# Optimization experiments

Hardware: AMD Instinct MI355X
Metric: run time of the kernel (lower is better)

The kernel has to match this reference:

```python
import jax, jax.numpy as jnp
import numpy as np
import math

D_MODEL = 1024
N_HEAD = 16
D_HEAD = D_MODEL // N_HEAD
B, T = 4, 2048


def setup_inputs() -> dict:
    key = jax.random.key(0)
    ks = jax.random.split(key, 9)
    x = jax.random.normal(ks[0], (B, T, D_MODEL), dtype=jnp.float32)
    # causal mask, broadcastable to [B, H, T, T]; mask==0 -> -1e9
    mask = jnp.tril(jnp.ones((T, T), dtype=bool))[None, None, :, :]
    # Xavier-uniform linear weights (stored as [in, out] for x @ W), zero biases
    limit = math.sqrt(6.0 / (D_MODEL + D_MODEL))
    def w(k):
        return jax.random.uniform(k, (D_MODEL, D_MODEL), dtype=jnp.float32, minval=-limit, maxval=limit)
    return {
        "x": x,
        "mask": mask,
        "wq": w(ks[1]), "bq": jnp.zeros((D_MODEL,), jnp.float32),
        "wk": w(ks[2]), "bk": jnp.zeros((D_MODEL,), jnp.float32),
        "wv": w(ks[3]), "bv": jnp.zeros((D_MODEL,), jnp.float32),
        "wo": w(ks[4]), "bo": jnp.zeros((D_MODEL,), jnp.float32),
    }


def reference(x, mask, wq, bq, wk, bk, wv, bv, wo, bo):
    b, t, c = x.shape
    h, dh = N_HEAD, D_HEAD
    # [B,T,C] -> [B,H,T,dh]
    def heads(y):
        return y.reshape(b, t, h, dh).transpose(0, 2, 1, 3)
    q = heads(x @ wq + bq)
    k = heads(x @ wk + bk)
    v = heads(x @ wv + bv)
    att = jnp.einsum("bhqd,bhkd->bhqk", q, k) / math.sqrt(dh)
    att = jnp.where(mask, att, jnp.float32(-1e9))
    att = jax.nn.softmax(att, axis=-1)  # dropout is identity in eval mode
    out = jnp.einsum("bhqk,bhkd->bhqd", att, v)
    out = out.transpose(0, 2, 1, 3).reshape(b, t, c)
    return out @ wo + bo
```

## Files before the change

kernel.cpp:

```cpp
#include <hip/hip_runtime.h>

typedef __bf16 bf16_t;
typedef bf16_t bf16x8 __attribute__((ext_vector_type(8)));
typedef bf16_t bf16x4 __attribute__((ext_vector_type(4)));
typedef float  f32x4  __attribute__((ext_vector_type(4)));
typedef float  f32x16 __attribute__((ext_vector_type(16)));
typedef unsigned int u32;
typedef u32 u32x2 __attribute__((ext_vector_type(2)));
typedef u32 u32x4 __attribute__((ext_vector_type(4)));

#define T_SEQ 2048
#define C_DIM 1024
#define NH    16
#define DH    64
#define BATCH 4
#define M_TOK (BATCH * T_SEQ)

#define Q_SCALE 0.1803368801111137f
#define DEFER_THR 8.0f

#define AS1 __attribute__((address_space(1)))
#define AS3 __attribute__((address_space(3)))

__device__ __forceinline__ void gld_lds16(const bf16_t* g, bf16_t* l) {
  __builtin_amdgcn_global_load_lds(
      (const AS1 u32*)(uintptr_t)g,
      (AS3 u32*)(u32)(uintptr_t)l, 16, 0, 0);
}

__device__ __forceinline__ void plswap(u32& a, u32& b) {
  u32x2 r = __builtin_amdgcn_permlane32_swap(a, b, false, false);
  a = r[0]; b = r[1];
}
__device__ __forceinline__ float xmax32(float x) {
  u32 a = __builtin_bit_cast(u32, x), b = a;
  plswap(a, b);
  return fmaxf(__builtin_bit_cast(float, a), __builtin_bit_cast(float, b));
}
__device__ __forceinline__ float xsum32(float x) {
  u32 a = __builtin_bit_cast(u32, x), b = a;
  plswap(a, b);
  return __builtin_bit_cast(float, a) + __builtin_bit_cast(float, b);
}

__global__ __launch_bounds__(256) void msa_cvt_x(const float* __restrict__ x,
                                                 bf16_t* __restrict__ xb, int n4) {
  int i = blockIdx.x * 256 + threadIdx.x;
  if (i < n4) {
    const float4 v = ((const float4*)x)[i];
    bf16x4 o;
    o[0] = (bf16_t)v.x; o[1] = (bf16_t)v.y; o[2] = (bf16_t)v.z; o[3] = (bf16_t)v.w;
    ((bf16x4*)xb)[i] = o;
  }
}

__global__ __launch_bounds__(256) void msa_transpose_w(
    const float* __restrict__ wq, const float* __restrict__ wk,
    const float* __restrict__ wv, const float* __restrict__ wo,
    bf16_t* __restrict__ wt_qkv, bf16_t* __restrict__ wt_o) {
  __shared__ float tile[32][33];
  const int a = blockIdx.z;
  const float* src = (a == 0) ? wq : (a == 1) ? wk : (a == 2) ? wv : wo;
  bf16_t* dst = (a < 3) ? (wt_qkv + (size_t)a * C_DIM * C_DIM) : wt_o;
  const int tx = threadIdx.x & 31, ty = threadIdx.x >> 5;
  const int bi = blockIdx.y * 32, bj = blockIdx.x * 32;
#pragma unroll
  for (int p = 0; p < 4; p++) {
    int r = p * 8 + ty;
    tile[r][tx] = src[(size_t)(bi + r) * C_DIM + bj + tx];
  }
  __syncthreads();
#pragma unroll
  for (int p = 0; p < 4; p++) {
    int r = p * 8 + ty;
    dst[(size_t)(bj + r) * C_DIM + bi + tx] = (bf16_t)tile[tx][r];
  }
}

__global__ __launch_bounds__(256) void msa_gemm_qkv(
    const bf16_t* __restrict__ xb, const bf16_t* __restrict__ wt,
    const float* __restrict__ bq, const float* __restrict__ bk,
    const float* __restrict__ bv,
    bf16_t* __restrict__ qo, bf16_t* __restrict__ ko, bf16_t* __restrict__ vto) {
  __shared__ bf16_t lA[2 * 128 * 32];
  __shared__ bf16_t lB[2 * 128 * 32];
  const int tid = threadIdx.x;
  const int w = tid >> 6, lane = tid & 63;
  const int lr = lane & 15, lg = lane >> 4;
  const int m0 = blockIdx.y * 128;
  const int n0 = blockIdx.x * 128;
  const int wm = (w >> 1) * 64, wn = (w & 1) * 64;

  const int srow = tid >> 2, scol = (tid & 3) * 8;
  const bf16_t* ga = xb + (size_t)(m0 + srow) * C_DIM + scol;
  const bf16_t* gb = wt + (size_t)(n0 + srow) * C_DIM + scol;

  f32x4 acc[4][4];
#pragma unroll
  for (int i = 0; i < 4; i++)
#pragma unroll
    for (int j = 0; j < 4; j++) acc[i][j] = (f32x4){0.f, 0.f, 0.f, 0.f};

  for (int k0 = 0; k0 < C_DIM; k0 += 64) {
    gld_lds16(ga + k0, &lA[tid * 8]);
    gld_lds16(ga + (size_t)64 * C_DIM + k0, &lA[2048 + tid * 8]);
    gld_lds16(ga + k0 + 32, &lA[4096 + tid * 8]);
    gld_lds16(ga + (size_t)64 * C_DIM + k0 + 32, &lA[6144 + tid * 8]);
    gld_lds16(gb + k0, &lB[tid * 8]);
    gld_lds16(gb + (size_t)64 * C_DIM + k0, &lB[2048 + tid * 8]);
    gld_lds16(gb + k0 + 32, &lB[4096 + tid * 8]);
    gld_lds16(gb + (size_t)64 * C_DIM + k0 + 32, &lB[6144 + tid * 8]);
    __syncthreads();
#pragma unroll
    for (int h = 0; h < 2; h++) {
      bf16x8 a[4], b[4];
#pragma unroll
      for (int mb = 0; mb < 4; mb++)
        a[mb] = *(const bf16x8*)&lA[h * 4096 + (wm + mb * 16 + lr) * 32 + lg * 8];
#pragma unroll
      for (int nb = 0; nb < 4; nb++)
        b[nb] = *(const bf16x8*)&lB[h * 4096 + (wn + nb * 16 + lr) * 32 + lg * 8];
#pragma unroll
      for (int mb = 0; mb < 4; mb++)
#pragma unroll
        for (int nb = 0; nb < 4; nb++)
          acc[mb][nb] = __builtin_amdgcn_mfma_f32_16x16x32_bf16(a[mb], b[nb], acc[mb][nb], 0, 0, 0);
    }
    __syncthreads();
  }

#pragma unroll
  for (int nb = 0; nb < 4; nb++) {
    const int n = n0 + wn + nb * 16 + lr;
    const int g = n >> 10, c = n & 1023, h = c >> 6, d = c & 63;
    const float bias = (g == 0) ? bq[c] : (g == 1) ? bk[c] : bv[c];
#pragma unroll
    for (int mb = 0; mb < 4; mb++) {
#pragma unroll
      for (int r = 0; r < 4; r++) {
        const int m = m0 + wm + mb * 16 + lg * 4 + r;
        const int bi = m >> 11, t = m & (T_SEQ - 1);
        float v = acc[mb][nb][r] + bias;
        if (g == 0)
          qo[(((size_t)bi * NH + h) * T_SEQ + t) * DH + d] = (bf16_t)(v * Q_SCALE);
        else if (g == 1)
          ko[(((size_t)bi * NH + h) * T_SEQ + t) * DH + d] = (bf16_t)v;
        else
          vto[(((size_t)bi * NH + h) * DH + d) * T_SEQ + t] = (bf16_t)v;
      }
    }
  }
}

__device__ __forceinline__ void pack_frag(const f32x16& s, bf16x8& pa0, bf16x8& pa1) {
  u32 pk8[8];
#pragma unroll
  for (int i = 0; i < 8; i++) {
    const unsigned short lo = __builtin_bit_cast(unsigned short, (bf16_t)s[2 * i]);
    const unsigned short hh = __builtin_bit_cast(unsigned short, (bf16_t)s[2 * i + 1]);
    pk8[i] = ((u32)hh << 16) | (u32)lo;
  }
  u32 f0w0 = pk8[0], f0w2 = pk8[2];
  u32 f0w1 = pk8[1], f0w3 = pk8[3];
  u32 f1w0 = pk8[4], f1w2 = pk8[6];
  u32 f1w1 = pk8[5], f1w3 = pk8[7];
  plswap(f0w0, f0w2);
  plswap(f0w1, f0w3);
  plswap(f1w0, f1w2);
  plswap(f1w1, f1w3);
  const u32x4 q0v = {f0w0, f0w1, f0w2, f0w3};
  const u32x4 q1v = {f1w0, f1w1, f1w2, f1w3};
  pa0 = __builtin_bit_cast(bf16x8, q0v);
  pa1 = __builtin_bit_cast(bf16x8, q1v);
}

__device__ __forceinline__ void sm_pack(f32x16& s, float& m_run, float& l_run,
                                        f32x16& o0, f32x16& o1,
                                        bf16x8& pa0, bf16x8& pa1) {
  float t0 = fmaxf(fmaxf(s[0], s[1]), s[2]);
  float t1 = fmaxf(fmaxf(s[3], s[4]), s[5]);
  float t2 = fmaxf(fmaxf(s[6], s[7]), s[8]);
  float t3 = fmaxf(fmaxf(s[9], s[10]), s[11]);
  float t4 = fmaxf(fmaxf(s[12], s[13]), s[14]);
  float t5 = fmaxf(fmaxf(t0, t1), s[15]);
  float mt = fmaxf(fmaxf(fmaxf(t2, t3), t4), t5);
  mt = xmax32(mt);

  if (__any(mt > m_run + DEFER_THR)) {
    const float mnew = fmaxf(m_run, mt);
    const float al = __builtin_amdgcn_exp2f(m_run - mnew);
    m_run = mnew;
    l_run *= al;
#pragma unroll
    for (int r = 0; r < 16; r++) { o0[r] *= al; o1[r] *= al; }
  }

#pragma unroll
  for (int r = 0; r < 16; r++) s[r] = __builtin_amdgcn_exp2f(s[r] - m_run);
  {
    float a0 = (s[0] + s[1]) + (s[2] + s[3]);
    float a1 = (s[4] + s[5]) + (s[6] + s[7]);
    float a2 = (s[8] + s[9]) + (s[10] + s[11]);
    float a3 = (s[12] + s[13]) + (s[14] + s[15]);
    l_run += xsum32((a0 + a1) + (a2 + a3));
  }
  pack_frag(s, pa0, pa1);
}

__device__ __forceinline__ void store_o(f32x16& o0, f32x16& o1, float l_fin,
                                        bf16_t* __restrict__ orow, const int hi) {
  const float inv = 1.0f / l_fin;
#pragma unroll
  for (int db = 0; db < 2; db++) {
#pragma unroll
    for (int r = 0; r < 16; r += 2) {
      const int d = db * 32 + (r & 3) + 8 * (r >> 2) + 4 * hi;
      const float v0 = (db ? o1[r] : o0[r]) * inv;
      const float v1 = (db ? o1[r + 1] : o0[r + 1]) * inv;
      const unsigned short b0 = __builtin_bit_cast(unsigned short, (bf16_t)v0);
      const unsigned short b1 = __builtin_bit_cast(unsigned short, (bf16_t)v1);
      *reinterpret_cast<u32*>(orow + d) = ((u32)b1 << 16) | (u32)b0;
    }
  }
}

__global__ __launch_bounds__(256, 2) void msa_attn_lds(
    const bf16_t* __restrict__ Q, const bf16_t* __restrict__ K,
    const bf16_t* __restrict__ Vt, bf16_t* __restrict__ O) {
  __shared__ __align__(16) char lds[16384];
  const int tid = threadIdx.x;
  const int w = tid >> 6;
  const int lane = tid & 63;
  const int l31 = lane & 31;
  const int hi = lane >> 5;
  const int bh = blockIdx.x;
  const int pg = blockIdx.y;
  const int p = pg * 4 + w;
  const int tS = p, tL = 63 - p;
  const int q0S = tS * 32, q0L = tL * 32;
  const int KT_MAX = 63 - 4 * pg;

  const bf16_t* Qh = Q + (size_t)bh * T_SEQ * DH;
  const bf16_t* Kh = K + (size_t)bh * T_SEQ * DH;
  const bf16_t* Vh = Vt + (size_t)bh * DH * T_SEQ;

  bf16x8 qfL[4], qfS[4];
#pragma unroll
  for (int dc = 0; dc < 4; dc++) {
    qfL[dc] = *(const bf16x8*)(Qh + (size_t)(q0L + l31) * DH + dc * 16 + hi * 8);
    qfS[dc] = *(const bf16x8*)(Qh + (size_t)(q0S + l31) * DH + dc * 16 + hi * 8);
  }

  f32x16 oL0, oL1, oS0, oS1;
#pragma unroll
  for (int r = 0; r < 16; r++) { oL0[r] = 0.f; oL1[r] = 0.f; oS0[r] = 0.f; oS1[r] = 0.f; }
  float mL = -1e30f, lL = 0.f, mS = -1e30f, lS = 0.f;
  const f32x16 z16 = {};

  const int ksw = (l31 & 7) << 4;
  const int vsw = (l31 & 3) << 4;
  const int krow = tid >> 3;
  const int kce = ((16 * (tid & 7)) ^ ((krow & 7) << 4)) >> 1;
  const int vrow = tid >> 2;
  const int vce = ((16 * (tid & 3)) ^ ((vrow & 3) << 4)) >> 1;

#define STAGE(KT, BUF)                                                         \
  {                                                                            \
    const int jj = (KT) * 32;                                                  \
    bf16_t* base_ = (bf16_t*)(lds + (BUF) * 8192);                             \
    gld_lds16(Kh + (size_t)(jj + krow) * DH + kce, base_ + tid * 8);           \
    gld_lds16(Vh + (size_t)vrow * T_SEQ + jj + vce, base_ + 2048 + tid * 8);   \
  }

  STAGE(0, 0);
  __syncthreads();

  for (int kt = 0; kt <= KT_MAX; ++kt) {
    const int buf = kt & 1;
    if (kt < KT_MAX) STAGE(kt + 1, buf ^ 1);

    const bool doL = (kt <= tL);
    if (doL) {
      const char* kb = lds + buf * 8192;
      const char* vb = kb + 4096;
      bf16x8 kf[4];
#pragma unroll
      for (int dc = 0; dc < 4; dc++)
        kf[dc] = *(const bf16x8*)(kb + l31 * 128 + ((dc * 32 + hi * 16) ^ ksw));
      const bf16x8 vf00 = *(const bf16x8*)(vb + l31 * 64 + ((hi * 16) ^ vsw));
      const bf16x8 vf01 = *(const bf16x8*)(vb + l31 * 64 + ((32 + hi * 16) ^ vsw));
      const bf16x8 vf10 = *(const bf16x8*)(vb + (32 + l31) * 64 + ((hi * 16) ^ vsw));
      const bf16x8 vf11 = *(const bf16x8*)(vb + (32 + l31) * 64 + ((32 + hi * 16) ^ vsw));

      const bool doS = (kt <= tS);
      f32x16 sL = __builtin_amdgcn_mfma_f32_32x32x16_bf16(kf[0], qfL[0], z16, 0, 0, 0);
#pragma unroll
      for (int dc = 1; dc < 4; dc++)
        sL = __builtin_amdgcn_mfma_f32_32x32x16_bf16(kf[dc], qfL[dc], sL, 0, 0, 0);
      f32x16 sS;
      if (doS) {
        sS = __builtin_amdgcn_mfma_f32_32x32x16_bf16(kf[0], qfS[0], z16, 0, 0, 0);
#pragma unroll
        for (int dc = 1; dc < 4; dc++)
          sS = __builtin_amdgcn_mfma_f32_32x32x16_bf16(kf[dc], qfS[dc], sS, 0, 0, 0);
      }
      if (kt == tL) {
#pragma unroll
        for (int r = 0; r < 16; r++) {
          const int jrow = (r & 3) + 8 * (r >> 2) + 4 * hi;
          if (jrow > l31) sL[r] = -1e30f;
        }
      }
      if (kt == tS) {
#pragma unroll
        for (int r = 0; r < 16; r++) {
          const int jrow = (r & 3) + 8 * (r >> 2) + 4 * hi;
          if (jrow > l31) sS[r] = -1e30f;
        }
      }
      bf16x8 paL0, paL1;
      sm_pack(sL, mL, lL, oL0, oL1, paL0, paL1);
      oL0 = __builtin_amdgcn_mfma_f32_32x32x16_bf16(vf00, paL0, oL0, 0, 0, 0);
      oL1 = __builtin_amdgcn_mfma_f32_32x32x16_bf16(vf10, paL0, oL1, 0, 0, 0);
      oL0 = __builtin_amdgcn_mfma_f32_32x32x16_bf16(vf01, paL1, oL0, 0, 0, 0);
      oL1 = __builtin_amdgcn_mfma_f32_32x32x16_bf16(vf11, paL1, oL1, 0, 0, 0);
      if (doS) {
        bf16x8 paS0, paS1;
        sm_pack(sS, mS, lS, oS0, oS1, paS0, paS1);
        oS0 = __builtin_amdgcn_mfma_f32_32x32x16_bf16(vf00, paS0, oS0, 0, 0, 0);
        oS1 = __builtin_amdgcn_mfma_f32_32x32x16_bf16(vf10, paS0, oS1, 0, 0, 0);
        oS0 = __builtin_amdgcn_mfma_f32_32x32x16_bf16(vf01, paS1, oS0, 0, 0, 0);
        oS1 = __builtin_amdgcn_mfma_f32_32x32x16_bf16(vf11, paS1, oS1, 0, 0, 0);
      }
    }
    __syncthreads();
  }
#undef STAGE

  const int b = bh >> 4, h = bh & 15;
  store_o(oL0, oL1, lL, O + ((size_t)b * T_SEQ + q0L + l31) * C_DIM + h * DH, hi);
  store_o(oS0, oS1, lS, O + ((size_t)b * T_SEQ + q0S + l31) * C_DIM + h * DH, hi);
}

__global__ __launch_bounds__(256) void msa_gemm_out(
    const bf16_t* __restrict__ ab, const bf16_t* __restrict__ wt,
    const float* __restrict__ bo, float* __restrict__ out) {
  __shared__ bf16_t lA[2 * 128 * 32];
  __shared__ bf16_t lB[2 * 128 * 32];
  const int tid = threadIdx.x;
  const int w = tid >> 6, lane = tid & 63;
  const int lr = lane & 15, lg = lane >> 4;
  const int m0 = blockIdx.y * 128;
  const int n0 = blockIdx.x * 128;
  const int wm = (w >> 1) * 64, wn = (w & 1) * 64;

  const int srow = tid >> 2, scol = (tid & 3) * 8;
  const bf16_t* ga = ab + (size_t)(m0 + srow) * C_DIM + scol;
  const bf16_t* gb = wt + (size_t)(n0 + srow) * C_DIM + scol;

  f32x4 acc[4][4];
#pragma unroll
  for (int i = 0; i < 4; i++)
#pragma unroll
    for (int j = 0; j < 4; j++) acc[i][j] = (f32x4){0.f, 0.f, 0.f, 0.f};

  for (int k0 = 0; k0 < C_DIM; k0 += 64) {
    gld_lds16(ga + k0, &lA[tid * 8]);
    gld_lds16(ga + (size_t)64 * C_DIM + k0, &lA[2048 + tid * 8]);
    gld_lds16(ga + k0 + 32, &lA[4096 + tid * 8]);
    gld_lds16(ga + (size_t)64 * C_DIM + k0 + 32, &lA[6144 + tid * 8]);
    gld_lds16(gb + k0, &lB[tid * 8]);
    gld_lds16(gb + (size_t)64 * C_DIM + k0, &lB[2048 + tid * 8]);
    gld_lds16(gb + k0 + 32, &lB[4096 + tid * 8]);
    gld_lds16(gb + (size_t)64 * C_DIM + k0 + 32, &lB[6144 + tid * 8]);
    __syncthreads();
#pragma unroll
    for (int h = 0; h < 2; h++) {
      bf16x8 a[4], b[4];
#pragma unroll
      for (int mb = 0; mb < 4; mb++)
        a[mb] = *(const bf16x8*)&lA[h * 4096 + (wm + mb * 16 + lr) * 32 + lg * 8];
#pragma unroll
      for (int nb = 0; nb < 4; nb++)
        b[nb] = *(const bf16x8*)&lB[h * 4096 + (wn + nb * 16 + lr) * 32 + lg * 8];
#pragma unroll
      for (int mb = 0; mb < 4; mb++)
#pragma unroll
        for (int nb = 0; nb < 4; nb++)
          acc[mb][nb] = __builtin_amdgcn_mfma_f32_16x16x32_bf16(a[mb], b[nb], acc[mb][nb], 0, 0, 0);
    }
    __syncthreads();
  }

#pragma unroll
  for (int nb = 0; nb < 4; nb++) {
    const int n = n0 + wn + nb * 16 + lr;
    const float bias = bo[n];
#pragma unroll
    for (int mb = 0; mb < 4; mb++) {
#pragma unroll
      for (int r = 0; r < 4; r++) {
        const int m = m0 + wm + mb * 16 + lg * 4 + r;
        out[(size_t)m * C_DIM + n] = acc[mb][nb][r] + bias;
      }
    }
  }
}

extern "C" void kernel_launch(void* const* d_in, const int* in_sizes, int n_in,
                              void* d_out, int out_size, void* d_ws, size_t ws_size,
                              hipStream_t stream) {
  const float* x  = (const float*)d_in[0];
  const float* wq = (const float*)d_in[2];
  const float* bq = (const float*)d_in[3];
  const float* wk = (const float*)d_in[4];
  const float* bk = (const float*)d_in[5];
  const float* wv = (const float*)d_in[6];
  const float* bv = (const float*)d_in[7];
  const float* wo = (const float*)d_in[8];
  const float* bo = (const float*)d_in[9];

  char* ws = (char*)d_ws;
  bf16_t* xb     = (bf16_t*)(ws);
  bf16_t* wt_qkv = (bf16_t*)(ws + (16ull << 20));
  bf16_t* wt_o   = (bf16_t*)(ws + (22ull << 20));
  bf16_t* qb     = (bf16_t*)(ws + (24ull << 20));
  bf16_t* kb     = (bf16_t*)(ws + (40ull << 20));
  bf16_t* vtb    = (bf16_t*)(ws + (56ull << 20));
  bf16_t* attn_o = xb;

  const int n4 = M_TOK * C_DIM / 4;
  msa_cvt_x<<<n4 / 256, 256, 0, stream>>>(x, xb, n4);
  msa_transpose_w<<<dim3(32, 32, 4), 256, 0, stream>>>(wq, wk, wv, wo, wt_qkv, wt_o);
  msa_gemm_qkv<<<dim3(24, 64), 256, 0, stream>>>(xb, wt_qkv, bq, bk, bv, qb, kb, vtb);
  msa_attn_lds<<<dim3(64, 8), 256, 0, stream>>>(qb, kb, vtb, attn_o);
  msa_gemm_out<<<dim3(8, 64), 256, 0, stream>>>(attn_o, wt_o, bo, (float*)d_out);
}
```

Before: 191.0 us.

## Triple-buffer GEMM LDS loads with swizzled layout and prefetch two tiles ahead

Replaces the synchronous load-then-compute loop in the QKV and output projection GEMMs with a shared macro. The macro keeps three LDS stages of K=32, prefetches two tiles ahead with direct global-to-LDS loads, and waits on vmcnt with a single barrier per iteration. It also XOR-swizzles the LDS column layout to reduce bank conflicts, raises wave priority around the MFMA block, and adds an occupancy hint of three blocks per CU. The aim is to hide global memory latency and remove the double barrier per K step. The cost is more LDS per block and reliance on hand-written waitcnt counts for correctness.

```diff
diff --git a/kernel.cpp b/kernel.cpp
--- a/kernel.cpp
+++ b/kernel.cpp
@@ -77,57 +77,81 @@
   }
 }
 
-__global__ __launch_bounds__(256) void msa_gemm_qkv(
+#define GQ_BUF 16384
+
+#define GEMM_CORE(APTR, BPTR, NT)                                              \
+  __shared__ __align__(16) char lds[3 * GQ_BUF];                               \
+  const int tid = threadIdx.x;                                                 \
+  const int w = tid >> 6, lane = tid & 63;                                     \
+  const int lr = lane & 15, lg = lane >> 4;                                    \
+  const int m0 = blockIdx.y * 128;                                             \
+  const int n0 = blockIdx.x * 128;                                             \
+  const int wm = (w >> 1) * 64, wn = (w & 1) * 64;                             \
+  const int rsw = (lg * 16) ^ ((lr & 3) << 4);                                 \
+  int Aoff[4], Boff[4];                                                        \
+  _Pragma("unroll") for (int f = 0; f < 4; f++) {                              \
+    Aoff[f] = (wm + f * 16 + lr) * 64 + rsw;                                   \
+    Boff[f] = 8192 + (wn + f * 16 + lr) * 64 + rsw;                            \
+  }                                                                            \
+  const int idx0 = tid, idx1 = 256 + tid;                                      \
+  const int r0 = idx0 >> 2, c0 = ((idx0 & 3) ^ (r0 & 3)) * 8;                  \
+  const int r1 = idx1 >> 2, c1 = ((idx1 & 3) ^ (r1 & 3)) * 8;                  \
+  const bf16_t* gA0 = (APTR) + (size_t)(m0 + r0) * C_DIM + c0;                 \
+  const bf16_t* gA1 = (APTR) + (size_t)(m0 + r1) * C_DIM + c1;                 \
+  const bf16_t* gB0 = (BPTR) + (size_t)(n0 + r0) * C_DIM + c0;                 \
+  const bf16_t* gB1 = (BPTR) + (size_t)(n0 + r1) * C_DIM + c1;                 \
+  f32x4 acc[4][4];                                                             \
+  _Pragma("unroll") for (int i = 0; i < 4; i++)                                \
+    _Pragma("unroll") for (int j = 0; j < 4; j++)                              \
+      acc[i][j] = (f32x4){0.f, 0.f, 0.f, 0.f};                                 \
+  GSTG(0, 0);                                                                  \
+  GSTG(1, GQ_BUF);                                                             \
+  asm volatile("s_waitcnt vmcnt(4)" ::: "memory");                             \
+  __builtin_amdgcn_s_barrier();                                                \
+  __builtin_amdgcn_sched_barrier(0);                                           \
+  int cb = 0;                                                                  \
+  for (int kt = 0; kt < (NT); ++kt) {                                          \
+    const char* base = lds + cb * GQ_BUF;                                      \
+    bf16x8 a[4], b[4];                                                         \
+    _Pragma("unroll") for (int f = 0; f < 4; f++) {                            \
+      a[f] = *(const bf16x8*)(base + Aoff[f]);                                 \
+      b[f] = *(const bf16x8*)(base + Boff[f]);                                 \
+    }                                                                          \
+    if (kt < (NT)-2) {                                                         \
+      int sb = cb + 2; if (sb >= 3) sb -= 3;                                   \
+      GSTG(kt + 2, sb * GQ_BUF);                                               \
+    }                                                                          \
+    __builtin_amdgcn_s_setprio(1);                                             \
+    _Pragma("unroll") for (int mf = 0; mf < 4; mf++)                           \
+      _Pragma("unroll") for (int nf = 0; nf < 4; nf++)                         \
+        acc[mf][nf] = __builtin_amdgcn_mfma_f32_16x16x32_bf16(                 \
+            a[mf], b[nf], acc[mf][nf], 0, 0, 0);                               \
+    __builtin_amdgcn_s_setprio(0);                                             \
+    if (kt < (NT)-2) {                                                         \
+      asm volatile("s_waitcnt vmcnt(4)" ::: "memory");                         \
+    } else {                                                                   \
+      asm volatile("s_waitcnt vmcnt(0)" ::: "memory");                         \
+    }                                                                          \
+    __builtin_amdgcn_s_barrier();                                              \
+    __builtin_amdgcn_sched_barrier(0);                                         \
+    if (++cb == 3) cb = 0;                                                     \
+  }
+
+#define GSTG(KT, BB)                                                           \
+  {                                                                            \
+    bf16_t* d_ = (bf16_t*)(lds + (BB));                                        \
+    gld_lds16(gA0 + (KT) * 32, d_ + tid * 8);                                  \
+    gld_lds16(gA1 + (KT) * 32, d_ + 2048 + tid * 8);                           \
+    gld_lds16(gB0 + (KT) * 32, d_ + 4096 + tid * 8);                           \
+    gld_lds16(gB1 + (KT) * 32, d_ + 6144 + tid * 8);                           \
+  }
+
+__global__ __launch_bounds__(256, 3) void msa_gemm_qkv(
     const bf16_t* __restrict__ xb, const bf16_t* __restrict__ wt,
     const float* __restrict__ bq, const float* __restrict__ bk,
     const float* __restrict__ bv,
     bf16_t* __restrict__ qo, bf16_t* __restrict__ ko, bf16_t* __restrict__ vto) {
-  __shared__ bf16_t lA[2 * 128 * 32];
-  __shared__ bf16_t lB[2 * 128 * 32];
-  const int tid = threadIdx.x;
-  const int w = tid >> 6, lane = tid & 63;
-  const int lr = lane & 15, lg = lane >> 4;
-  const int m0 = blockIdx.y * 128;
-  const int n0 = blockIdx.x * 128;
-  const int wm = (w >> 1) * 64, wn = (w & 1) * 64;
-
-  const int srow = tid >> 2, scol = (tid & 3) * 8;
-  const bf16_t* ga = xb + (size_t)(m0 + srow) * C_DIM + scol;
-  const bf16_t* gb = wt + (size_t)(n0 + srow) * C_DIM + scol;
-
-  f32x4 acc[4][4];
-#pragma unroll
-  for (int i = 0; i < 4; i++)
-#pragma unroll
-    for (int j = 0; j < 4; j++) acc[i][j] = (f32x4){0.f, 0.f, 0.f, 0.f};
-
-  for (int k0 = 0; k0 < C_DIM; k0 += 64) {
-    gld_lds16(ga + k0, &lA[tid * 8]);
-    gld_lds16(ga + (size_t)64 * C_DIM + k0, &lA[2048 + tid * 8]);
-    gld_lds16(ga + k0 + 32, &lA[4096 + tid * 8]);
-    gld_lds16(ga + (size_t)64 * C_DIM + k0 + 32, &lA[6144 + tid * 8]);
-    gld_lds16(gb + k0, &lB[tid * 8]);
-    gld_lds16(gb + (size_t)64 * C_DIM + k0, &lB[2048 + tid * 8]);
-    gld_lds16(gb + k0 + 32, &lB[4096 + tid * 8]);
-    gld_lds16(gb + (size_t)64 * C_DIM + k0 + 32, &lB[6144 + tid * 8]);
-    __syncthreads();
-#pragma unroll
-    for (int h = 0; h < 2; h++) {
-      bf16x8 a[4], b[4];
-#pragma unroll
-      for (int mb = 0; mb < 4; mb++)
-        a[mb] = *(const bf16x8*)&lA[h * 4096 + (wm + mb * 16 + lr) * 32 + lg * 8];
-#pragma unroll
-      for (int nb = 0; nb < 4; nb++)
-        b[nb] = *(const bf16x8*)&lB[h * 4096 + (wn + nb * 16 + lr) * 32 + lg * 8];
-#pragma unroll
-      for (int mb = 0; mb < 4; mb++)
-#pragma unroll
-        for (int nb = 0; nb < 4; nb++)
-          acc[mb][nb] = __builtin_amdgcn_mfma_f32_16x16x32_bf16(a[mb], b[nb], acc[mb][nb], 0, 0, 0);
-    }
-    __syncthreads();
-  }
+  GEMM_CORE(xb, wt, 32)
 
 #pragma unroll
   for (int nb = 0; nb < 4; nb++) {
@@ -147,6 +171,26 @@
           ko[(((size_t)bi * NH + h) * T_SEQ + t) * DH + d] = (bf16_t)v;
         else
           vto[(((size_t)bi * NH + h) * DH + d) * T_SEQ + t] = (bf16_t)v;
+      }
+    }
+  }
+}
+
+__global__ __launch_bounds__(256, 3) void msa_gemm_out(
+    const bf16_t* __restrict__ ab, const bf16_t* __restrict__ wt,
+    const float* __restrict__ bo, float* __restrict__ out) {
+  GEMM_CORE(ab, wt, 32)
+
+#pragma unroll
+  for (int nb = 0; nb < 4; nb++) {
+    const int n = n0 + wn + nb * 16 + lr;
+    const float bias = bo[n];
+#pragma unroll
+    for (int mb = 0; mb < 4; mb++) {
+#pragma unroll
+      for (int r = 0; r < 4; r++) {
+        const int m = m0 + wm + mb * 16 + lg * 4 + r;
+        out[(size_t)m * C_DIM + n] = acc[mb][nb][r] + bias;
       }
     }
   }
@@ -342,71 +386,6 @@
   store_o(oS0, oS1, lS, O + ((size_t)b * T_SEQ + q0S + l31) * C_DIM + h * DH, hi);
 }
 
-__global__ __launch_bounds__(256) void msa_gemm_out(
-    const bf16_t* __restrict__ ab, const bf16_t* __restrict__ wt,
-    const float* __restrict__ bo, float* __restrict__ out) {
-  __shared__ bf16_t lA[2 * 128 * 32];
-  __shared__ bf16_t lB[2 * 128 * 32];
-  const int tid = threadIdx.x;
-  const int w = tid >> 6, lane = tid & 63;
-  const int lr = lane & 15, lg = lane >> 4;
-  const int m0 = blockIdx.y * 128;
-  const int n0 = blockIdx.x * 128;
-  const int wm = (w >> 1) * 64, wn = (w & 1) * 64;
-
-  const int srow = tid >> 2, scol = (tid & 3) * 8;
-  const bf16_t* ga = ab + (size_t)(m0 + srow) * C_DIM + scol;
-  const bf16_t* gb = wt + (size_t)(n0 + srow) * C_DIM + scol;
-
-  f32x4 acc[4][4];
-#pragma unroll
-  for (int i = 0; i < 4; i++)
-#pragma unroll
-    for (int j = 0; j < 4; j++) acc[i][j] = (f32x4){0.f, 0.f, 0.f, 0.f};
-
-  for (int k0 = 0; k0 < C_DIM; k0 += 64) {
-    gld_lds16(ga + k0, &lA[tid * 8]);
-    gld_lds16(ga + (size_t)64 * C_DIM + k0, &lA[2048 + tid * 8]);
-    gld_lds16(ga + k0 + 32, &lA[4096 + tid * 8]);
-    gld_lds16(ga + (size_t)64 * C_DIM + k0 + 32, &lA[6144 + tid * 8]);
-    gld_lds16(gb + k0, &lB[tid * 8]);
-    gld_lds16(gb + (size_t)64 * C_DIM + k0, &lB[2048 + tid * 8]);
-    gld_lds16(gb + k0 + 32, &lB[4096 + tid * 8]);
-    gld_lds16(gb + (size_t)64 * C_DIM + k0 + 32, &lB[6144 + tid * 8]);
-    __syncthreads();
-#pragma unroll
-    for (int h = 0; h < 2; h++) {
-      bf16x8 a[4], b[4];
-#pragma unroll
-      for (int mb = 0; mb < 4; mb++)
-        a[mb] = *(const bf16x8*)&lA[h * 4096 + (wm + mb * 16 + lr) * 32 + lg * 8];
-#pragma unroll
-      for (int nb = 0; nb < 4; nb++)
-        b[nb] = *(const bf16x8*)&lB[h * 4096 + (wn + nb * 16 + lr) * 32 + lg * 8];
-#pragma unroll
-      for (int mb = 0; mb < 4; mb++)
-#pragma unroll
-        for (int nb = 0; nb < 4; nb++)
-          acc[mb][nb] = __builtin_amdgcn_mfma_f32_16x16x32_bf16(a[mb], b[nb], acc[mb][nb], 0, 0, 0);
-    }
-    __syncthreads();
-  }
-
-#pragma unroll
-  for (int nb = 0; nb < 4; nb++) {
-    const int n = n0 + wn + nb * 16 + lr;
-    const float bias = bo[n];
-#pragma unroll
-    for (int mb = 0; mb < 4; mb++) {
-#pragma unroll
-      for (int r = 0; r < 4; r++) {
-        const int m = m0 + wm + mb * 16 + lg * 4 + r;
-        out[(size_t)m * C_DIM + n] = acc[mb][nb][r] + bias;
-      }
-    }
-  }
-}
-
 extern "C" void kernel_launch(void* const* d_in, const int* in_sizes, int n_in,
                               void* d_out, int out_size, void* d_ws, size_t ws_size,
                               hipStream_t stream) {
```

New measurement: 187.3 us. About the same (-2.0%).
